# Kernel tuning notes

Measured on AMD Instinct MI355X. Metric: run time of the kernel, lower is better.

Reference implementation:

```python
import jax, jax.numpy as jnp
import numpy as np

B, D, C = 4096, 1024, 5000
ALPHA, BETA = 1.0, 0.5


def setup_inputs() -> dict:
    key = jax.random.key(0)
    ks = jax.random.split(key, 7)
    return {
        "anchor": jax.random.normal(ks[0], (B, D), dtype=jnp.float32),
        "positive": jax.random.normal(ks[1], (B, D), dtype=jnp.float32),
        "negative": jax.random.normal(ks[2], (B, D), dtype=jnp.float32),
        "outputs": jax.random.normal(ks[3], (3 * B, C), dtype=jnp.float32),
        "labels_anchor": jax.random.randint(ks[4], (B,), 0, C, dtype=jnp.int64),
        "labels_neg": jax.random.randint(ks[5], (B,), 0, C, dtype=jnp.int64),
        "exemplars": jax.random.normal(ks[6], (C, D), dtype=jnp.float32),
    }


def reference(anchor, positive, negative, outputs, labels_anchor, labels_neg, exemplars):
    # Cross-entropy over [3B, C] logits with concatenated labels (mean reduction)
    labels = jnp.concatenate([labels_anchor, labels_anchor, labels_neg], axis=0)
    logp = jax.nn.log_softmax(outputs, axis=-1)
    loss_softmax = -jnp.mean(jnp.take_along_axis(logp, labels[:, None], axis=1))

    # Batched L2 distances anchor -> all exemplars via |a|^2 + |e|^2 - 2 a.e
    a2 = jnp.sum(anchor * anchor, axis=-1, keepdims=True)          # [B,1]
    e2 = jnp.sum(exemplars * exemplars, axis=-1)                   # [C]
    sq = a2 + e2[None, :] - 2.0 * (anchor @ exemplars.T)           # [B,C]
    d_all = jnp.sqrt(jnp.maximum(sq, 0.0))

    d_ref = jnp.take_along_axis(d_all, labels_anchor[:, None], axis=1)[:, 0]  # [B]
    d_closest = jnp.min(d_all, axis=1)                                        # [B]

    tp = jnp.sqrt(jnp.sum((anchor - positive) ** 2, axis=-1))  # [B]
    tn = jnp.sqrt(jnp.sum((anchor - negative) ** 2, axis=-1))  # [B]

    loss_triplet = jnp.sum(jax.nn.relu(tp - tn)).reshape(1)
    loss_center = jnp.sum(jax.nn.relu(d_ref - d_closest)).reshape(1)
    loss_total = loss_softmax + ALPHA * loss_triplet + BETA * loss_center
    return (loss_total, loss_triplet, loss_softmax, loss_center)
```

## Files before the change

kernel.cpp:

```cpp
#include <hip/hip_runtime.h>
#include <hip/hip_bf16.h>

typedef unsigned short u16;
typedef __bf16 bf16x8 __attribute__((ext_vector_type(8)));
typedef float f32x4 __attribute__((ext_vector_type(4)));

#define B_ 4096
#define D_ 1024
#define C_ 5000
#define NPAD 5120
#define THREE_B 12288

__device__ __forceinline__ float wave_red_sum(float v) {
#pragma unroll
  for (int off = 32; off; off >>= 1) v += __shfl_down(v, off, 64);
  return v;
}

__device__ __forceinline__ u16 f2bf(float f) {
  __bf16 h = (__bf16)f;
  return __builtin_bit_cast(u16, h);
}

__device__ __forceinline__ void gld_lds16(const u16* g, u16* l) {
  __builtin_amdgcn_global_load_lds(
      (const __attribute__((address_space(1))) unsigned int*)g,
      (__attribute__((address_space(3))) unsigned int*)l, 16, 0, 0);
}

__global__ __launch_bounds__(256) void conv_kernel(
    const float* __restrict__ anchor, const float* __restrict__ positive,
    const float* __restrict__ negative, const float* __restrict__ ex,
    u16* __restrict__ Abf, u16* __restrict__ Ebf, float* __restrict__ a2,
    float* __restrict__ e2, float* __restrict__ trip) {
  int tid = threadIdx.x;
  if (blockIdx.x < B_) {
    int r = blockIdx.x;
    const float4* a4 = (const float4*)(anchor + (size_t)r * D_);
    const float4* p4 = (const float4*)(positive + (size_t)r * D_);
    const float4* n4 = (const float4*)(negative + (size_t)r * D_);
    float4 a = a4[tid], p = p4[tid], n = n4[tid];
    float sa = a.x * a.x + a.y * a.y + a.z * a.z + a.w * a.w;
    float dx = a.x - p.x, dy = a.y - p.y, dz = a.z - p.z, dw = a.w - p.w;
    float sp = dx * dx + dy * dy + dz * dz + dw * dw;
    dx = a.x - n.x; dy = a.y - n.y; dz = a.z - n.z; dw = a.w - n.w;
    float sn = dx * dx + dy * dy + dz * dz + dw * dw;
    ushort4 o;
    o.x = f2bf(a.x); o.y = f2bf(a.y); o.z = f2bf(a.z); o.w = f2bf(a.w);
    ((ushort4*)(Abf + (size_t)r * D_))[tid] = o;
    __shared__ float red[3][4];
    sa = wave_red_sum(sa); sp = wave_red_sum(sp); sn = wave_red_sum(sn);
    if (!(tid & 63)) { int w = tid >> 6; red[0][w] = sa; red[1][w] = sp; red[2][w] = sn; }
    __syncthreads();
    if (tid == 0) {
      float ta = red[0][0] + red[0][1] + red[0][2] + red[0][3];
      float tp = red[1][0] + red[1][1] + red[1][2] + red[1][3];
      float tn = red[2][0] + red[2][1] + red[2][2] + red[2][3];
      a2[r] = ta;
      trip[r] = fmaxf(sqrtf(tp) - sqrtf(tn), 0.0f);
    }
  } else {
    int r = blockIdx.x - B_;
    if (r < C_) {
      const float4* e4 = (const float4*)(ex + (size_t)r * D_);
      float4 e = e4[tid];
      float se = e.x * e.x + e.y * e.y + e.z * e.z + e.w * e.w;
      ushort4 o;
      o.x = f2bf(e.x); o.y = f2bf(e.y); o.z = f2bf(e.z); o.w = f2bf(e.w);
      ((ushort4*)(Ebf + (size_t)r * D_))[tid] = o;
      __shared__ float red2[4];
      se = wave_red_sum(se);
      if (!(tid & 63)) red2[tid >> 6] = se;
      __syncthreads();
      if (tid == 0) e2[r] = red2[0] + red2[1] + red2[2] + red2[3];
    } else {
      ushort4 z; z.x = 0; z.y = 0; z.z = 0; z.w = 0;
      ((ushort4*)(Ebf + (size_t)r * D_))[tid] = z;
      if (tid == 0) e2[r] = 0.0f;
    }
  }
}

__global__ __launch_bounds__(256) void ce_kernel(
    const float* __restrict__ outputs, const int* __restrict__ la,
    const int* __restrict__ ln, float* __restrict__ ce_row) {
  int row_id = (blockIdx.x << 2) + (threadIdx.x >> 6);
  int lane = threadIdx.x & 63;
  const float* row = outputs + (size_t)row_id * C_;
  const float4* row4 = (const float4*)row;
  const float LOG2E = 1.4426950408889634f;
  float s = 0.0f;
#pragma unroll
  for (int k = 0; k < 19; ++k) {
    float4 v = row4[lane + (k << 6)];
    s += __builtin_amdgcn_exp2f(v.x * LOG2E) + __builtin_amdgcn_exp2f(v.y * LOG2E) +
         __builtin_amdgcn_exp2f(v.z * LOG2E) + __builtin_amdgcn_exp2f(v.w * LOG2E);
  }
  if (lane < 34) {
    float4 v = row4[lane + 19 * 64];
    s += __builtin_amdgcn_exp2f(v.x * LOG2E) + __builtin_amdgcn_exp2f(v.y * LOG2E) +
         __builtin_amdgcn_exp2f(v.z * LOG2E) + __builtin_amdgcn_exp2f(v.w * LOG2E);
  }
  s = wave_red_sum(s);
  if (lane == 0) {
    int label = (row_id < 2 * B_) ? la[row_id & (B_ - 1)] : ln[row_id - 2 * B_];
    ce_row[row_id] = 0.69314718055994531f * __builtin_amdgcn_logf(s) - row[label];
  }
}

#define BM 128
#define BN 128
#define BK 64
__global__ __launch_bounds__(256, 3) void gemm_min_kernel(
    const u16* __restrict__ Abf, const u16* __restrict__ Ebf,
    const float* __restrict__ a2, const float* __restrict__ e2,
    const int* __restrict__ labels, float* __restrict__ dmin,
    float* __restrict__ dref) {
  __shared__ alignas(16) u16 As[BM * BK];
  __shared__ alignas(16) u16 Bs[BN * BK];
  __shared__ int lab_s[BM];
  __shared__ float a2_s[BM];
  __shared__ float e2_s[BN];

  const int tid = threadIdx.x;
  const int bm = blockIdx.x;
  const int bn = blockIdx.y;
  const int lane = tid & 63;
  const int wv = tid >> 6;
  const int wm = wv >> 1, wn = wv & 1;
  const int quad = lane >> 4, l15 = lane & 15;

  if (tid < BM) {
    lab_s[tid] = labels[bm * BM + tid];
    a2_s[tid] = a2[bm * BM + tid];
  } else {
    e2_s[tid - 128] = e2[bn * BN + (tid - 128)];
  }

  f32x4 acc[4][4];
  f32x4 zero4 = {0.0f, 0.0f, 0.0f, 0.0f};
#pragma unroll
  for (int i = 0; i < 4; ++i)
#pragma unroll
    for (int j = 0; j < 4; ++j) acc[i][j] = zero4;

  const u16* Ag = Abf + (size_t)(bm * BM) * D_;
  const u16* Eg = Ebf + (size_t)(bn * BN) * D_;

  for (int k0 = 0; k0 < D_; k0 += BK) {
    __syncthreads();
#pragma unroll
    for (int t = 0; t < 4; ++t) {
      int id = t * 256 + tid;
      int row = id >> 3, cz = id & 7;
      int kc = cz ^ (row & 7);
      gld_lds16(Ag + (size_t)row * D_ + k0 + kc * 8, &As[id * 8]);
    }
#pragma unroll
    for (int t = 0; t < 4; ++t) {
      int id = t * 256 + tid;
      int row = id >> 3, cz = id & 7;
      int kc = cz ^ (row & 7);
      gld_lds16(Eg + (size_t)row * D_ + k0 + kc * 8, &Bs[id * 8]);
    }
    __syncthreads();
#pragma unroll
    for (int ks = 0; ks < 2; ++ks) {
      bf16x8 af[4], bfr[4];
#pragma unroll
      for (int i = 0; i < 4; ++i) {
        int r = wm * 64 + i * 16 + l15;
        int sw = (ks * 4 + quad) ^ (l15 & 7);
        af[i] = *(const bf16x8*)&As[r * BK + sw * 8];
      }
#pragma unroll
      for (int j = 0; j < 4; ++j) {
        int r = wn * 64 + j * 16 + l15;
        int sw = (ks * 4 + quad) ^ (l15 & 7);
        bfr[j] = *(const bf16x8*)&Bs[r * BK + sw * 8];
      }
#pragma unroll
      for (int i = 0; i < 4; ++i)
#pragma unroll
        for (int j = 0; j < 4; ++j)
          acc[i][j] = __builtin_amdgcn_mfma_f32_16x16x32_bf16(af[i], bfr[j],
                                                              acc[i][j], 0, 0, 0);
    }
  }

#pragma unroll
  for (int i = 0; i < 4; ++i) {
    int rbase = wm * 64 + i * 16 + quad * 4;
#pragma unroll
    for (int reg = 0; reg < 4; ++reg) {
      int rloc = rbase + reg;
      int m = bm * BM + rloc;
      float a2m = a2_s[rloc];
      int lab = lab_s[rloc];
      float dmn = 3.0e38f;
#pragma unroll
      for (int j = 0; j < 4; ++j) {
        int nloc = wn * 64 + j * 16 + l15;
        int n = bn * BN + nloc;
        float dot = acc[i][j][reg];
        float sq = a2m + e2_s[nloc] - 2.0f * dot;
        float d = sqrtf(fmaxf(sq, 0.0f));
        if (n < C_) {
          dmn = fminf(dmn, d);
          if (n == lab) dref[m] = d;
        }
      }
#pragma unroll
      for (int msk = 1; msk < 16; msk <<= 1)
        dmn = fminf(dmn, __shfl_xor(dmn, msk, 64));
      if (l15 == 0)
        atomicMin((unsigned int*)&dmin[m], __float_as_uint(dmn));
    }
  }
}

__global__ __launch_bounds__(256) void final_kernel(
    const float* __restrict__ ce_row, const float* __restrict__ trip,
    const float* __restrict__ dmin, const float* __restrict__ dref,
    float* __restrict__ out) {
  int tid = threadIdx.x;
  float sc = 0.0f, st = 0.0f, sce = 0.0f;
  for (int r = tid; r < B_; r += 256) {
    sc += fmaxf(dref[r] - dmin[r], 0.0f);
    st += trip[r];
  }
  for (int r = tid; r < THREE_B; r += 256) sce += ce_row[r];
  __shared__ float red[3][4];
  sc = wave_red_sum(sc); st = wave_red_sum(st); sce = wave_red_sum(sce);
  if (!(tid & 63)) { int w = tid >> 6; red[0][w] = sc; red[1][w] = st; red[2][w] = sce; }
  __syncthreads();
  if (tid == 0) {
    float center = red[0][0] + red[0][1] + red[0][2] + red[0][3];
    float triplet = red[1][0] + red[1][1] + red[1][2] + red[1][3];
    float softmax_mean =
        (red[2][0] + red[2][1] + red[2][2] + red[2][3]) / (float)THREE_B;
    out[0] = softmax_mean + 1.0f * triplet + 0.5f * center;
    out[1] = triplet;
    out[2] = softmax_mean;
    out[3] = center;
  }
}

extern "C" void kernel_launch(void* const* d_in, const int* in_sizes, int n_in,
                              void* d_out, int out_size, void* d_ws, size_t ws_size,
                              hipStream_t stream) {
  const float* anchor = (const float*)d_in[0];
  const float* positive = (const float*)d_in[1];
  const float* negative = (const float*)d_in[2];
  const float* outputs = (const float*)d_in[3];
  const int* la = (const int*)d_in[4];
  const int* ln = (const int*)d_in[5];
  const float* exemplars = (const float*)d_in[6];
  float* out = (float*)d_out;

  float* ws_f = (float*)d_ws;
  float* a2 = ws_f;
  float* e2 = a2 + B_;
  float* dmin = e2 + NPAD;
  float* dref = dmin + B_;
  float* ce_row = dref + B_;
  float* trip = ce_row + THREE_B;
  u16* Abf = (u16*)(trip + B_);
  u16* Ebf = Abf + (size_t)B_ * D_;

  hipMemsetAsync(dmin, 0x7F, B_ * sizeof(float), stream);

  conv_kernel<<<B_ + NPAD, 256, 0, stream>>>(anchor, positive, negative,
                                             exemplars, Abf, Ebf, a2, e2, trip);
  gemm_min_kernel<<<dim3(32, 40), 256, 0, stream>>>(Abf, Ebf, a2, e2, la, dmin, dref);
  ce_kernel<<<THREE_B / 4, 256, 0, stream>>>(outputs, la, ln, ce_row);
  final_kernel<<<1, 256, 0, stream>>>(ce_row, trip, dmin, dref, out);
}
```

Before: 457.6 us.

## Switch distance GEMM to FP8 MFMA and fuse CE into GEMM launch

Quantizes anchor and exemplar rows to FP8 with a pre-permuted, swizzled layout and runs the distance GEMM with fp8 MFMA. This halves operand bytes and doubles MFMA throughput. The cross-entropy blocks are merged into the GEMM launch so both workloads run concurrently. The memset is folded into the conversion kernel, and the final reduction uses 1024 threads. FP8 quantization of the dot products can shift the nearest-exemplar distances enough to break accuracy tolerances.

```diff
diff --git a/kernel.cpp b/kernel.cpp
--- a/kernel.cpp
+++ b/kernel.cpp
@@ -2,14 +2,17 @@
 #include <hip/hip_bf16.h>
 
 typedef unsigned short u16;
-typedef __bf16 bf16x8 __attribute__((ext_vector_type(8)));
+typedef unsigned char u8;
 typedef float f32x4 __attribute__((ext_vector_type(4)));
+typedef long l2 __attribute__((ext_vector_type(2)));
 
 #define B_ 4096
 #define D_ 1024
 #define C_ 5000
 #define NPAD 5120
 #define THREE_B 12288
+#define GEMM_BLOCKS 1280
+#define CE_BLOCKS 3072
 
 __device__ __forceinline__ float wave_red_sum(float v) {
 #pragma unroll
@@ -17,22 +20,31 @@
   return v;
 }
 
-__device__ __forceinline__ u16 f2bf(float f) {
-  __bf16 h = (__bf16)f;
-  return __builtin_bit_cast(u16, h);
-}
-
-__device__ __forceinline__ void gld_lds16(const u16* g, u16* l) {
+__device__ __forceinline__ void gld_lds16(const u8* g, u8* l) {
   __builtin_amdgcn_global_load_lds(
       (const __attribute__((address_space(1))) unsigned int*)g,
       (__attribute__((address_space(3))) unsigned int*)l, 16, 0, 0);
 }
 
+__device__ __forceinline__ int pk_fp8(float4 a) {
+  int r = __builtin_amdgcn_cvt_pk_fp8_f32(a.x, a.y, 0, false);
+  r = __builtin_amdgcn_cvt_pk_fp8_f32(a.z, a.w, r, true);
+  return r;
+}
+
+__device__ __forceinline__ int perm_pos(int tid, int r) {
+  int kt = tid >> 4;
+  int ks = (tid >> 3) & 1;
+  int quad = (tid >> 1) & 3;
+  int c = quad ^ ((r >> 1) & 3);
+  return kt * 64 + c * 16 + ks * 8 + ((tid & 1) << 2);
+}
+
 __global__ __launch_bounds__(256) void conv_kernel(
     const float* __restrict__ anchor, const float* __restrict__ positive,
     const float* __restrict__ negative, const float* __restrict__ ex,
-    u16* __restrict__ Abf, u16* __restrict__ Ebf, float* __restrict__ a2,
-    float* __restrict__ e2, float* __restrict__ trip) {
+    u8* __restrict__ Abf, u8* __restrict__ Ebf, float* __restrict__ a2,
+    float* __restrict__ e2, float* __restrict__ trip, float* __restrict__ dmin) {
   int tid = threadIdx.x;
   if (blockIdx.x < B_) {
     int r = blockIdx.x;
@@ -45,19 +57,17 @@
     float sp = dx * dx + dy * dy + dz * dz + dw * dw;
     dx = a.x - n.x; dy = a.y - n.y; dz = a.z - n.z; dw = a.w - n.w;
     float sn = dx * dx + dy * dy + dz * dz + dw * dw;
-    ushort4 o;
-    o.x = f2bf(a.x); o.y = f2bf(a.y); o.z = f2bf(a.z); o.w = f2bf(a.w);
-    ((ushort4*)(Abf + (size_t)r * D_))[tid] = o;
+    *(int*)(Abf + (size_t)r * D_ + perm_pos(tid, r)) = pk_fp8(a);
     __shared__ float red[3][4];
     sa = wave_red_sum(sa); sp = wave_red_sum(sp); sn = wave_red_sum(sn);
     if (!(tid & 63)) { int w = tid >> 6; red[0][w] = sa; red[1][w] = sp; red[2][w] = sn; }
     __syncthreads();
     if (tid == 0) {
-      float ta = red[0][0] + red[0][1] + red[0][2] + red[0][3];
+      a2[r] = red[0][0] + red[0][1] + red[0][2] + red[0][3];
       float tp = red[1][0] + red[1][1] + red[1][2] + red[1][3];
       float tn = red[2][0] + red[2][1] + red[2][2] + red[2][3];
-      a2[r] = ta;
       trip[r] = fmaxf(sqrtf(tp) - sqrtf(tn), 0.0f);
+      dmin[r] = 3.3e38f;
     }
   } else {
     int r = blockIdx.x - B_;
@@ -65,66 +75,65 @@
       const float4* e4 = (const float4*)(ex + (size_t)r * D_);
       float4 e = e4[tid];
       float se = e.x * e.x + e.y * e.y + e.z * e.z + e.w * e.w;
-      ushort4 o;
-      o.x = f2bf(e.x); o.y = f2bf(e.y); o.z = f2bf(e.z); o.w = f2bf(e.w);
-      ((ushort4*)(Ebf + (size_t)r * D_))[tid] = o;
+      *(int*)(Ebf + (size_t)r * D_ + perm_pos(tid, r)) = pk_fp8(e);
       __shared__ float red2[4];
       se = wave_red_sum(se);
       if (!(tid & 63)) red2[tid >> 6] = se;
       __syncthreads();
       if (tid == 0) e2[r] = red2[0] + red2[1] + red2[2] + red2[3];
     } else {
-      ushort4 z; z.x = 0; z.y = 0; z.z = 0; z.w = 0;
-      ((ushort4*)(Ebf + (size_t)r * D_))[tid] = z;
+      *(int*)(Ebf + (size_t)r * D_ + tid * 4) = 0;
       if (tid == 0) e2[r] = 0.0f;
     }
-  }
-}
-
-__global__ __launch_bounds__(256) void ce_kernel(
-    const float* __restrict__ outputs, const int* __restrict__ la,
-    const int* __restrict__ ln, float* __restrict__ ce_row) {
-  int row_id = (blockIdx.x << 2) + (threadIdx.x >> 6);
-  int lane = threadIdx.x & 63;
-  const float* row = outputs + (size_t)row_id * C_;
-  const float4* row4 = (const float4*)row;
-  const float LOG2E = 1.4426950408889634f;
-  float s = 0.0f;
-#pragma unroll
-  for (int k = 0; k < 19; ++k) {
-    float4 v = row4[lane + (k << 6)];
-    s += __builtin_amdgcn_exp2f(v.x * LOG2E) + __builtin_amdgcn_exp2f(v.y * LOG2E) +
-         __builtin_amdgcn_exp2f(v.z * LOG2E) + __builtin_amdgcn_exp2f(v.w * LOG2E);
-  }
-  if (lane < 34) {
-    float4 v = row4[lane + 19 * 64];
-    s += __builtin_amdgcn_exp2f(v.x * LOG2E) + __builtin_amdgcn_exp2f(v.y * LOG2E) +
-         __builtin_amdgcn_exp2f(v.z * LOG2E) + __builtin_amdgcn_exp2f(v.w * LOG2E);
-  }
-  s = wave_red_sum(s);
-  if (lane == 0) {
-    int label = (row_id < 2 * B_) ? la[row_id & (B_ - 1)] : ln[row_id - 2 * B_];
-    ce_row[row_id] = 0.69314718055994531f * __builtin_amdgcn_logf(s) - row[label];
   }
 }
 
 #define BM 128
 #define BN 128
-#define BK 64
-__global__ __launch_bounds__(256, 3) void gemm_min_kernel(
-    const u16* __restrict__ Abf, const u16* __restrict__ Ebf,
+#define BKB 64
+__global__ __launch_bounds__(256, 3) void gemm_ce_kernel(
+    const u8* __restrict__ Abf, const u8* __restrict__ Ebf,
     const float* __restrict__ a2, const float* __restrict__ e2,
     const int* __restrict__ labels, float* __restrict__ dmin,
-    float* __restrict__ dref) {
-  __shared__ alignas(16) u16 As[BM * BK];
-  __shared__ alignas(16) u16 Bs[BN * BK];
+    float* __restrict__ dref, const float* __restrict__ outputs,
+    const int* __restrict__ la, const int* __restrict__ ln,
+    float* __restrict__ ce_row) {
+  __shared__ alignas(16) u8 As[BM * BKB];
+  __shared__ alignas(16) u8 Bs[BN * BKB];
   __shared__ int lab_s[BM];
   __shared__ float a2_s[BM];
   __shared__ float e2_s[BN];
 
   const int tid = threadIdx.x;
-  const int bm = blockIdx.x;
-  const int bn = blockIdx.y;
+
+  if (blockIdx.x >= GEMM_BLOCKS) {
+    int row_id = ((blockIdx.x - GEMM_BLOCKS) << 2) + (tid >> 6);
+    int lane = tid & 63;
+    const float* row = outputs + (size_t)row_id * C_;
+    const float4* row4 = (const float4*)row;
+    const float LOG2E = 1.4426950408889634f;
+    float s = 0.0f;
+#pragma unroll
+    for (int k = 0; k < 19; ++k) {
+      float4 v = row4[lane + (k << 6)];
+      s += __builtin_amdgcn_exp2f(v.x * LOG2E) + __builtin_amdgcn_exp2f(v.y * LOG2E) +
+           __builtin_amdgcn_exp2f(v.z * LOG2E) + __builtin_amdgcn_exp2f(v.w * LOG2E);
+    }
+    if (lane < 34) {
+      float4 v = row4[lane + 19 * 64];
+      s += __builtin_amdgcn_exp2f(v.x * LOG2E) + __builtin_amdgcn_exp2f(v.y * LOG2E) +
+           __builtin_amdgcn_exp2f(v.z * LOG2E) + __builtin_amdgcn_exp2f(v.w * LOG2E);
+    }
+    s = wave_red_sum(s);
+    if (lane == 0) {
+      int label = (row_id < 2 * B_) ? la[row_id & (B_ - 1)] : ln[row_id - 2 * B_];
+      ce_row[row_id] = 0.69314718055994531f * __builtin_amdgcn_logf(s) - row[label];
+    }
+    return;
+  }
+
+  const int bm = blockIdx.x & 31;
+  const int bn = blockIdx.x >> 5;
   const int lane = tid & 63;
   const int wv = tid >> 6;
   const int wm = wv >> 1, wn = wv & 1;
@@ -144,48 +153,48 @@
 #pragma unroll
     for (int j = 0; j < 4; ++j) acc[i][j] = zero4;
 
-  const u16* Ag = Abf + (size_t)(bm * BM) * D_;
-  const u16* Eg = Ebf + (size_t)(bn * BN) * D_;
-
-  for (int k0 = 0; k0 < D_; k0 += BK) {
+  const u8* Ag = Abf + (size_t)(bm * BM) * D_;
+  const u8* Eg = Ebf + (size_t)(bn * BN) * D_;
+
+  for (int k0 = 0; k0 < D_; k0 += BKB) {
     __syncthreads();
 #pragma unroll
-    for (int t = 0; t < 4; ++t) {
+    for (int t = 0; t < 2; ++t) {
       int id = t * 256 + tid;
-      int row = id >> 3, cz = id & 7;
-      int kc = cz ^ (row & 7);
-      gld_lds16(Ag + (size_t)row * D_ + k0 + kc * 8, &As[id * 8]);
-    }
-#pragma unroll
-    for (int t = 0; t < 4; ++t) {
+      gld_lds16(Ag + (size_t)(id >> 2) * D_ + k0 + (id & 3) * 16, &As[id * 16]);
+    }
+#pragma unroll
+    for (int t = 0; t < 2; ++t) {
       int id = t * 256 + tid;
-      int row = id >> 3, cz = id & 7;
-      int kc = cz ^ (row & 7);
-      gld_lds16(Eg + (size_t)row * D_ + k0 + kc * 8, &Bs[id * 8]);
+      gld_lds16(Eg + (size_t)(id >> 2) * D_ + k0 + (id & 3) * 16, &Bs[id * 16]);
     }
     __syncthreads();
-#pragma unroll
-    for (int ks = 0; ks < 2; ++ks) {
-      bf16x8 af[4], bfr[4];
-#pragma unroll
-      for (int i = 0; i < 4; ++i) {
-        int r = wm * 64 + i * 16 + l15;
-        int sw = (ks * 4 + quad) ^ (l15 & 7);
-        af[i] = *(const bf16x8*)&As[r * BK + sw * 8];
-      }
-#pragma unroll
-      for (int j = 0; j < 4; ++j) {
-        int r = wn * 64 + j * 16 + l15;
-        int sw = (ks * 4 + quad) ^ (l15 & 7);
-        bfr[j] = *(const bf16x8*)&Bs[r * BK + sw * 8];
-      }
-#pragma unroll
-      for (int i = 0; i < 4; ++i)
-#pragma unroll
-        for (int j = 0; j < 4; ++j)
-          acc[i][j] = __builtin_amdgcn_mfma_f32_16x16x32_bf16(af[i], bfr[j],
-                                                              acc[i][j], 0, 0, 0);
-    }
+
+    l2 af[4], bfr[4];
+#pragma unroll
+    for (int i = 0; i < 4; ++i) {
+      int r = wm * 64 + i * 16 + l15;
+      int c = quad ^ ((r >> 1) & 3);
+      af[i] = *(const l2*)&As[r * BKB + c * 16];
+    }
+#pragma unroll
+    for (int j = 0; j < 4; ++j) {
+      int r = wn * 64 + j * 16 + l15;
+      int c = quad ^ ((r >> 1) & 3);
+      bfr[j] = *(const l2*)&Bs[r * BKB + c * 16];
+    }
+#pragma unroll
+    for (int i = 0; i < 4; ++i)
+#pragma unroll
+      for (int j = 0; j < 4; ++j)
+        acc[i][j] = __builtin_amdgcn_mfma_f32_16x16x32_fp8_fp8(
+            af[i].x, bfr[j].x, acc[i][j], 0, 0, 0);
+#pragma unroll
+    for (int i = 0; i < 4; ++i)
+#pragma unroll
+      for (int j = 0; j < 4; ++j)
+        acc[i][j] = __builtin_amdgcn_mfma_f32_16x16x32_fp8_fp8(
+            af[i].y, bfr[j].y, acc[i][j], 0, 0, 0);
   }
 
 #pragma unroll
@@ -219,26 +228,26 @@
   }
 }
 
-__global__ __launch_bounds__(256) void final_kernel(
+__global__ __launch_bounds__(1024) void final_kernel(
     const float* __restrict__ ce_row, const float* __restrict__ trip,
     const float* __restrict__ dmin, const float* __restrict__ dref,
     float* __restrict__ out) {
   int tid = threadIdx.x;
   float sc = 0.0f, st = 0.0f, sce = 0.0f;
-  for (int r = tid; r < B_; r += 256) {
+  for (int r = tid; r < B_; r += 1024) {
     sc += fmaxf(dref[r] - dmin[r], 0.0f);
     st += trip[r];
   }
-  for (int r = tid; r < THREE_B; r += 256) sce += ce_row[r];
-  __shared__ float red[3][4];
+  for (int r = tid; r < THREE_B; r += 1024) sce += ce_row[r];
+  __shared__ float red[3][16];
   sc = wave_red_sum(sc); st = wave_red_sum(st); sce = wave_red_sum(sce);
   if (!(tid & 63)) { int w = tid >> 6; red[0][w] = sc; red[1][w] = st; red[2][w] = sce; }
   __syncthreads();
   if (tid == 0) {
-    float center = red[0][0] + red[0][1] + red[0][2] + red[0][3];
-    float triplet = red[1][0] + red[1][1] + red[1][2] + red[1][3];
-    float softmax_mean =
-        (red[2][0] + red[2][1] + red[2][2] + red[2][3]) / (float)THREE_B;
+    float center = 0.0f, triplet = 0.0f, smx = 0.0f;
+#pragma unroll
+    for (int w = 0; w < 16; ++w) { center += red[0][w]; triplet += red[1][w]; smx += red[2][w]; }
+    float softmax_mean = smx / (float)THREE_B;
     out[0] = softmax_mean + 1.0f * triplet + 0.5f * center;
     out[1] = triplet;
     out[2] = softmax_mean;
@@ -265,14 +274,12 @@
   float* dref = dmin + B_;
   float* ce_row = dref + B_;
   float* trip = ce_row + THREE_B;
-  u16* Abf = (u16*)(trip + B_);
-  u16* Ebf = Abf + (size_t)B_ * D_;
-
-  hipMemsetAsync(dmin, 0x7F, B_ * sizeof(float), stream);
+  u8* Abf = (u8*)(trip + B_);
+  u8* Ebf = Abf + (size_t)B_ * D_;
 
   conv_kernel<<<B_ + NPAD, 256, 0, stream>>>(anchor, positive, negative,
-                                             exemplars, Abf, Ebf, a2, e2, trip);
-  gemm_min_kernel<<<dim3(32, 40), 256, 0, stream>>>(Abf, Ebf, a2, e2, la, dmin, dref);
-  ce_kernel<<<THREE_B / 4, 256, 0, stream>>>(outputs, la, ln, ce_row);
-  final_kernel<<<1, 256, 0, stream>>>(ce_row, trip, dmin, dref, out);
-}
+                                             exemplars, Abf, Ebf, a2, e2, trip, dmin);
+  gemm_ce_kernel<<<GEMM_BLOCKS + CE_BLOCKS, 256, 0, stream>>>(
+      Abf, Ebf, a2, e2, la, dmin, dref, outputs, la, ln, ce_row);
+  final_kernel<<<1, 1024, 0, stream>>>(ce_row, trip, dmin, dref, out);
+}
```

Result: faster. 411.2 us (-10.1%).
